# Performance work log

Hardware: AMD Instinct MI355X
Metric: run time of the kernel (lower is better)

Reference implementation:

```python
import jax, jax.numpy as jnp
from jax import lax
import numpy as np

DEPTH = 4
D_MODEL = 192
D_INNER = 384
D_STATE = 16
D_CONV = 4
DT_RANK = 12
STRIDE = 4
NUM_PATCHES = 400
L_SEQ = NUM_PATCHES + 1  # +1 cls token appended at the end
EPS = 1e-5


def _rmsnorm(x, w):
    x = x.astype(jnp.float32)
    return (x * lax.rsqrt(jnp.mean(x * x, axis=-1, keepdims=True) + EPS)) * w


def _mamba(x, in_w, cw, cb, xp_w, dtw, dtb, A_log, Dv, ow):
    # x: [B, L, D_MODEL]
    B = x.shape[0]
    xz = jnp.einsum('bld,ed->ble', x, in_w)            # [B, L, 2*D_INNER]
    u, z = jnp.split(xz, 2, axis=-1)                   # [B, L, D_INNER] each
    # causal depthwise conv over L
    u_t = jnp.transpose(u, (0, 2, 1))                  # [B, D_INNER, L]
    u_pad = jnp.pad(u_t, ((0, 0), (0, 0), (D_CONV - 1, 0)))
    conv = lax.conv_general_dilated(
        u_pad, cw[:, None, :], (1,), 'VALID',
        dimension_numbers=('NCH', 'OIH', 'NCH'),
        feature_group_count=D_INNER)                   # [B, D_INNER, L]
    u = jax.nn.silu(conv + cb[:, None])
    u = jnp.transpose(u, (0, 2, 1))                    # [B, L, D_INNER]
    xdbl = jnp.einsum('bld,ed->ble', u, xp_w)          # [B, L, 44]
    dt, Bm, Cm = jnp.split(xdbl, [DT_RANK, DT_RANK + D_STATE], axis=-1)
    dt = jax.nn.softplus(jnp.einsum('blr,dr->bld', dt, dtw) + dtb)  # [B, L, D_INNER]
    A = -jnp.exp(A_log)                                # [D_INNER, D_STATE]
    dA = jnp.exp(dt[..., None] * A)                    # [B, L, D_INNER, D_STATE]
    dBu = dt[..., None] * Bm[:, :, None, :] * u[..., None]
    h0 = jnp.zeros((B, D_INNER, D_STATE), dtype=dA.dtype)

    def step(h, inp):
        dA_t, dBu_t = inp
        h = dA_t * h + dBu_t
        return h, h

    _, hs = lax.scan(step, h0, (jnp.swapaxes(dA, 0, 1), jnp.swapaxes(dBu, 0, 1)))
    hs = jnp.swapaxes(hs, 0, 1)                        # [B, L, D_INNER, D_STATE]
    y = jnp.einsum('bldn,bln->bld', hs, Cm) + u * Dv
    y = y * jax.nn.silu(z)
    return jnp.einsum('bld,ed->ble', y, ow)            # [B, L, D_MODEL]


def _forward(imgs, patch_w, patch_b, pos_embed, cls_token, norm_w, in_proj_w,
             conv_w, conv_b, xproj_w, dt_w, dt_b, A_log, D_param, out_w,
             normf_w, head_w, head_b):
    B = imgs.shape[0]
    # StrideEmbed: non-overlapping strides of 4 bytes -> linear to embed_dim
    x = imgs.reshape(B, NUM_PATCHES, STRIDE) @ patch_w + patch_b  # [B, 400, 192]
    x = x + pos_embed[:, :-1, :]
    cls = cls_token + pos_embed[:, -1:, :]             # [1, 1, 192]
    x = jnp.concatenate([x, jnp.broadcast_to(cls, (B, 1, D_MODEL))], axis=1)
    hidden = x
    residual = None
    for i in range(DEPTH):
        residual = hidden if residual is None else hidden + residual  # fp32 residual stream
        h = _rmsnorm(residual, norm_w[i])
        hidden = _mamba(h, in_proj_w[i], conv_w[i], conv_b[i], xproj_w[i],
                        dt_w[i], dt_b[i], A_log[i], D_param[i], out_w[i])
    x = _rmsnorm(hidden + residual, normf_w)
    cls_out = x[:, -1, :]                              # [B, 192]
    logits = cls_out @ head_w.T + head_b               # [B, 1000]
    return logits


def setup_inputs() -> dict:
    key = jax.random.key(0)
    ks = jax.random.split(key, 16)
    B = 32
    rn = lambda k, s, sc: jax.random.normal(k, s, dtype=jnp.float32) * sc
    A_log = jnp.broadcast_to(jnp.log(jnp.arange(1.0, D_STATE + 1.0, dtype=jnp.float32)),
                             (DEPTH, D_INNER, D_STATE))
    return {
        'imgs': rn(ks[0], (B, 1, 40, 40), 1.0),
        'patch_w': rn(ks[1], (STRIDE, D_MODEL), 0.1),
        'patch_b': jnp.zeros((D_MODEL,), jnp.float32),
        'pos_embed': rn(ks[2], (1, L_SEQ, D_MODEL), 0.02),
        'cls_token': rn(ks[3], (1, 1, D_MODEL), 0.02),
        'norm_w': jnp.ones((DEPTH, D_MODEL), jnp.float32),
        'in_proj_w': rn(ks[4], (DEPTH, 2 * D_INNER, D_MODEL), 0.05),
        'conv_w': rn(ks[5], (DEPTH, D_INNER, D_CONV), 0.3),
        'conv_b': jnp.zeros((DEPTH, D_INNER), jnp.float32),
        'xproj_w': rn(ks[6], (DEPTH, DT_RANK + 2 * D_STATE, D_INNER), 0.05),
        'dt_w': rn(ks[7], (DEPTH, D_INNER, DT_RANK), 0.1),
        'dt_b': rn(ks[8], (DEPTH, D_INNER), 0.5) - 4.0,
        'A_log': A_log,
        'D_param': jnp.ones((DEPTH, D_INNER), jnp.float32),
        'out_w': rn(ks[9], (DEPTH, D_MODEL, D_INNER), 0.05),
        'normf_w': jnp.ones((D_MODEL,), jnp.float32),
        'head_w': rn(ks[10], (1000, D_MODEL), 0.05),
        'head_b': jnp.zeros((1000,), jnp.float32),
    }


def reference(imgs, patch_w, patch_b, pos_embed, cls_token, norm_w, in_proj_w,
              conv_w, conv_b, xproj_w, dt_w, dt_b, A_log, D_param, out_w,
              normf_w, head_w, head_b):
    return _forward(imgs, patch_w, patch_b, pos_embed, cls_token, norm_w,
                    in_proj_w, conv_w, conv_b, xproj_w, dt_w, dt_b, A_log,
                    D_param, out_w, normf_w, head_w, head_b)
```

## Files before the change

kernel.cpp:

```cpp
#include <hip/hip_runtime.h>
#include <hip/hip_bf16.h>

#define B_SZ 32
#define LSEQ 401
#define NT (B_SZ * LSEQ)
#define DM 192
#define DI 384
#define DS 16
#define EPSF 1e-5f
#define ST 40
#define STP 44
#define NCH 8
#define PQN 1376256

typedef __attribute__((ext_vector_type(8))) short short8;
typedef __attribute__((ext_vector_type(4))) float f32x4;
typedef __hip_bfloat16 bf16;

#define OFF_IMGS    0
#define OFF_PATCHW  51200
#define OFF_PATCHB  51968
#define OFF_POS     52160
#define OFF_CLS     129152
#define OFF_NORMW   129344
#define OFF_INW     130112
#define OFF_CONVW   719936
#define OFF_CONVB   726080
#define OFF_XPROJW  727616
#define OFF_DTW     795200
#define OFF_DTB     813632
#define OFF_ALOG    815168
#define OFF_DP      839744
#define OFF_OUTW    841280
#define OFF_NORMF   1136192
#define OFF_HEADW   1136384
#define OFF_HEADB   1328384
#define OFF_TOTAL   1329384

#define WB_INW   0
#define WB_XPJ   589824
#define WB_OUT   688128
#define WB_DTW   983040
#define WB_TOTAL 1032192

__device__ __forceinline__ int chunk_s(int c) { return c == 0 ? 0 : c * 50 + 1; }
__device__ __forceinline__ int chunk_e(int c) { return (c + 1) * 50 + 1; }

__device__ __forceinline__ float ldsrc(const void* p, int off, int isbf) {
  return isbf ? __bfloat162float(((const bf16*)p)[off]) : ((const float*)p)[off];
}
__device__ __forceinline__ float fast_silu(float z) {
  return z * __builtin_amdgcn_rcpf(1.f + __expf(-z));
}
__device__ __forceinline__ float fast_softplus(float x) {
  float e = __expf(x);
  return (x > 15.f) ? x : __logf(1.f + e);
}

#define DPP_ADD(x, ctrl) \
  x += __int_as_float(__builtin_amdgcn_update_dpp(0, __float_as_int(x), ctrl, 0xF, 0xF, true))
__device__ __forceinline__ float row_sum16(float x) {
  DPP_ADD(x, 0xB1);
  DPP_ADD(x, 0x4E);
  DPP_ADD(x, 0x124);
  DPP_ADD(x, 0x128);
  return x;
}

struct P18 { const void* p[18]; };

__global__ __launch_bounds__(256) void k_convwb(P18 t, float* __restrict__ fin,
                                                bf16* __restrict__ wb) {
  static const int st[19] = {OFF_IMGS, OFF_PATCHW, OFF_PATCHB, OFF_POS, OFF_CLS,
                             OFF_NORMW, OFF_INW, OFF_CONVW, OFF_CONVB, OFF_XPROJW,
                             OFF_DTW, OFF_DTB, OFF_ALOG, OFF_DP, OFF_OUTW,
                             OFF_NORMF, OFF_HEADW, OFF_HEADB, OFF_TOTAL};
  int isbf = (((const unsigned short*)t.p[5])[0] == 0x3F80) ? 1 : 0;
  int idx = blockIdx.x * 256 + threadIdx.x;
  if (idx < OFF_TOTAL) {
    int lo = 0;
#pragma unroll
    for (int i = 1; i < 18; ++i) if (idx >= st[i]) lo = i;
    fin[idx] = ldsrc(t.p[lo], idx - st[lo], isbf);
  } else if (idx < OFF_TOTAL + WB_TOTAL) {
    int j = idx - OFF_TOTAL;
    float v;
    if (j < WB_XPJ) {
      v = ldsrc(t.p[6], j, isbf);
    } else if (j < WB_OUT) {
      int i2 = j - WB_XPJ;
      int l = i2 / (64 * 384);
      int r = (i2 / 384) & 63;
      int k = i2 % 384;
      v = (r < 44) ? ldsrc(t.p[9], l * 44 * 384 + r * 384 + k, isbf) : 0.f;
    } else if (j < WB_DTW) {
      v = ldsrc(t.p[14], j - WB_OUT, isbf);
    } else {
      int i2 = j - WB_DTW;
      int l = i2 / (384 * 32);
      int r = i2 % (384 * 32);
      int d = r >> 5;
      int k = r & 31;
      v = (k < 12) ? ldsrc(t.p[10], l * 4608 + d * 12 + k, isbf) : 0.f;
    }
    wb[j] = __float2bfloat16(v);
  }
}

__device__ __forceinline__ void inproj32(const bf16 (*shb)[200],
                                         const bf16* __restrict__ Win,
                                         bf16* __restrict__ xb,
                                         bf16* __restrict__ zb,
                                         int row0, int tid) {
  int lane = tid & 63, wave = tid >> 6;
  int q = lane >> 4, mlo = lane & 15;
  short8 afrA[6], afrB[6];
#pragma unroll
  for (int kk = 0; kk < 6; ++kk) {
    afrA[kk] = *(const short8*)&shb[mlo][kk * 32 + q * 8];
    afrB[kk] = *(const short8*)&shb[16 + mlo][kk * 32 + q * 8];
  }
  const bf16* wbase = Win + (size_t)(wave * 96 + mlo) * DM + q * 8;
  short8 bc[6];
#pragma unroll
  for (int kk = 0; kk < 6; ++kk) bc[kk] = *(const short8*)(wbase + kk * 32);
#pragma unroll
  for (int j = 0; j < 6; ++j) {
    short8 bn[6];
    if (j < 5) {
#pragma unroll
      for (int kk = 0; kk < 6; ++kk)
        bn[kk] = *(const short8*)(wbase + (size_t)(j + 1) * 16 * DM + kk * 32);
    }
    f32x4 aA = {}, aB = {};
#pragma unroll
    for (int kk = 0; kk < 6; ++kk) {
      aA = __builtin_amdgcn_mfma_f32_16x16x32_bf16(afrA[kk], bc[kk], aA, 0, 0, 0);
      aB = __builtin_amdgcn_mfma_f32_16x16x32_bf16(afrB[kk], bc[kk], aB, 0, 0, 0);
    }
    int n = wave * 96 + j * 16 + mlo;
    if (n < DI) {
#pragma unroll
      for (int i = 0; i < 4; ++i) {
        xb[(size_t)(row0 + q * 4 + i) * DI + n] = __float2bfloat16(aA[i]);
        xb[(size_t)(row0 + 16 + q * 4 + i) * DI + n] = __float2bfloat16(aB[i]);
      }
    } else {
      int nz = n - DI;
#pragma unroll
      for (int i = 0; i < 4; ++i) {
        zb[(size_t)(row0 + q * 4 + i) * DI + nz] = __float2bfloat16(aA[i]);
        zb[(size_t)(row0 + 16 + q * 4 + i) * DI + nz] = __float2bfloat16(aB[i]);
      }
    }
    if (j < 5) {
#pragma unroll
      for (int kk = 0; kk < 6; ++kk) bc[kk] = bn[kk];
    }
  }
}

__global__ __launch_bounds__(512) void k_embedin(const float* __restrict__ fin,
                                                 float* __restrict__ residual,
                                                 const bf16* __restrict__ Win,
                                                 bf16* __restrict__ xb,
                                                 bf16* __restrict__ zb) {
  __shared__ bf16 shb[32][200];
  const float* imgs = fin + OFF_IMGS;
  const float* pw   = fin + OFF_PATCHW;
  const float* pb   = fin + OFF_PATCHB;
  const float* pos  = fin + OFF_POS;
  const float* cls  = fin + OFF_CLS;
  const float* nw0  = fin + OFF_NORMW;
  int tid = threadIdx.x;
  int row0 = blockIdx.x * 32;
  {
    int row = tid >> 4, g = tid & 15;
    int t = row0 + row;
    int b = t / LSEQ, l = t % LSEQ;
    float im[4];
    if (l < 400) {
#pragma unroll
      for (int s = 0; s < 4; ++s) im[s] = imgs[b * 1600 + l * 4 + s];
    }
    float rn[12], ss = 0.f;
#pragma unroll
    for (int k = 0; k < 12; ++k) {
      int col = g + 16 * k;
      float v;
      if (l < 400) {
        v = pb[col] + pos[l * DM + col];
#pragma unroll
        for (int s = 0; s < 4; ++s) v = fmaf(im[s], pw[s * DM + col], v);
      } else {
        v = cls[col] + pos[400 * DM + col];
      }
      residual[(size_t)t * DM + col] = v;
      rn[k] = v;
      ss = fmaf(v, v, ss);
    }
    ss = row_sum16(ss);
    float sres = rsqrtf(ss / (float)DM + EPSF);
#pragma unroll
    for (int k = 0; k < 12; ++k) {
      int col = g + 16 * k;
      shb[row][col] = __float2bfloat16(rn[k] * sres * nw0[col]);
    }
  }
  __syncthreads();
  inproj32(shb, Win, xb, zb, row0, tid);
}

__global__ __launch_bounds__(512) void k_xdt(const bf16* __restrict__ xb,
                                             const float* __restrict__ cw,
                                             const float* __restrict__ cb,
                                             const bf16* __restrict__ Wbf,
                                             float* __restrict__ xdbl,
                                             const bf16* __restrict__ dtwb,
                                             const float* __restrict__ dtb,
                                             bf16* __restrict__ ub,
                                             bf16* __restrict__ dto) {
  __shared__ bf16  sxt[19][392];
  __shared__ bf16  su[16][392];
  __shared__ float4 scw4[384];
  __shared__ float scb[384];
  __shared__ float sxp[2][16][48];
  __shared__ bf16  sxb[16][32];
  int row0 = blockIdx.x * 16;
  int tid = threadIdx.x;
  for (int i = tid; i < 19 * 48; i += 512) {
    int r = i / 48, c8 = i - r * 48;
    int t = row0 - 3 + r;
    if (t < 0) t = 0;
    *(short8*)&sxt[r][c8 * 8] = *(const short8*)(xb + (size_t)t * DI + c8 * 8);
  }
  for (int i = tid; i < 384; i += 512) {
    scw4[i] = ((const float4*)cw)[i];
    scb[i] = cb[i];
  }
  __syncthreads();
  for (int i = tid; i < 768; i += 512) {
    int tok = i / 48;
    int c8 = i - tok * 48;
    int d0 = c8 * 8;
    int t = row0 + tok;
    int l = t % LSEQ;
    float xr[4][8];
#pragma unroll
    for (int k = 0; k < 4; ++k) {
      short8 v = *(const short8*)&sxt[tok + k][d0];
      bool ok = (l - 3 + k) >= 0;
#pragma unroll
      for (int j = 0; j < 8; ++j) {
        unsigned int uu = ((unsigned int)(unsigned short)v[j]) << 16;
        xr[k][j] = ok ? __uint_as_float(uu) : 0.f;
      }
    }
    short8 uvv;
#pragma unroll
    for (int j = 0; j < 8; ++j) {
      float4 w = scw4[d0 + j];
      float a = scb[d0 + j];
      a = fmaf(xr[0][j], w.x, a);
      a = fmaf(xr[1][j], w.y, a);
      a = fmaf(xr[2][j], w.z, a);
      a = fmaf(xr[3][j], w.w, a);
      bf16 h = __float2bfloat16(fast_silu(a));
      uvv[j] = *reinterpret_cast<short*>(&h);
    }
    *(short8*)&su[tok][d0] = uvv;
    *(short8*)(ub + (size_t)t * DI + d0) = uvv;
  }
  __syncthreads();
  int lane = tid & 63;
  int wave = tid >> 6;
  int q = lane >> 4;
  int mlo = lane & 15;
  if (wave < 6) {
    int colw = (wave % 3) * 16;
    int kh = wave / 3;
    f32x4 acc = {};
    for (int k0 = 0; k0 < 192; k0 += 32) {
      short8 a = *(const short8*)&su[mlo][kh * 192 + k0 + q * 8];
      short8 b = *(const short8*)(Wbf + (size_t)(colw + mlo) * DI + kh * 192 + k0 + q * 8);
      acc = __builtin_amdgcn_mfma_f32_16x16x32_bf16(a, b, acc, 0, 0, 0);
    }
#pragma unroll
    for (int i = 0; i < 4; ++i) sxp[kh][q * 4 + i][colw + mlo] = acc[i];
  }
  __syncthreads();
  for (int i = tid; i < 16 * 44; i += 512) {
    int r = i / 44, c = i - r * 44;
    xdbl[(size_t)(row0 + r) * 44 + c] = sxp[0][r][c] + sxp[1][r][c];
  }
  for (int i = tid; i < 512; i += 512) {
    int tok = i >> 5, k = i & 31;
    sxb[tok][k] = __float2bfloat16(k < 12 ? sxp[0][tok][k] + sxp[1][tok][k] : 0.f);
  }
  __syncthreads();
  short8 afrag = *(const short8*)&sxb[mlo][q * 8];
#pragma unroll
  for (int jt = 0; jt < 3; ++jt) {
    int d = (wave * 3 + jt) * 16 + mlo;
    short8 bfrag = *(const short8*)(dtwb + (size_t)d * 32 + q * 8);
    f32x4 acc = {};
    acc = __builtin_amdgcn_mfma_f32_16x16x32_bf16(afrag, bfrag, acc, 0, 0, 0);
    float dtbv = dtb[d];
#pragma unroll
    for (int i = 0; i < 4; ++i)
      dto[(size_t)(row0 + q * 4 + i) * DI + d] =
          __float2bfloat16(fast_softplus(acc[i] + dtbv));
  }
}

__global__ __launch_bounds__(512) void k_scanA(const bf16* __restrict__ ub,
                                               const bf16* __restrict__ dtv,
                                               const float* __restrict__ xdbl,
                                               const float* __restrict__ A_log,
                                               float* __restrict__ Pq) {
  __shared__ float sdt[32][STP], sw[32][STP], sB[16][STP];
  int bx = blockIdx.x, b = blockIdx.y, c = blockIdx.z;
  int d0 = bx * 32;
  int tid = threadIdx.x;
  int dloc = tid >> 4, n = tid & 15;
  float A = -__expf(A_log[(d0 + dloc) * DS + n]);
  float S = 0.f, h = 0.f;
  int base = b * LSEQ;
  int lt = tid >> 5, lj = tid & 31;
  int s = chunk_s(c), e = chunk_e(c);
  for (int t0 = s; t0 < e; t0 += ST) {
    int tc = min(ST, e - t0);
    for (int tt = lt; tt < tc; tt += 16) {
      int g = base + t0 + tt;
      float dv = __bfloat162float(dtv[(size_t)g * DI + d0 + lj]);
      sdt[lj][tt] = dv;
      sw[lj][tt] = dv * __bfloat162float(ub[(size_t)g * DI + d0 + lj]);
      if (lj < 16) sB[lj][tt] = xdbl[(size_t)g * 44 + 12 + lj];
    }
    __syncthreads();
    int l4 = 0;
    for (; l4 + 4 <= tc; l4 += 4) {
      float4 dt4 = *(const float4*)&sdt[dloc][l4];
      float4 w4  = *(const float4*)&sw[dloc][l4];
      float4 B4  = *(const float4*)&sB[n][l4];
      h = fmaf(__expf(dt4.x * A), h, w4.x * B4.x);
      h = fmaf(__expf(dt4.y * A), h, w4.y * B4.y);
      h = fmaf(__expf(dt4.z * A), h, w4.z * B4.z);
      h = fmaf(__expf(dt4.w * A), h, w4.w * B4.w);
      S += dt4.x + dt4.y + dt4.z + dt4.w;
    }
    for (; l4 < tc; ++l4) {
      float dv = sdt[dloc][l4];
      h = fmaf(__expf(dv * A), h, sw[dloc][l4] * sB[n][l4]);
      S += dv;
    }
    __syncthreads();
  }
  int idx = ((c * B_SZ + b) * 12 + bx) * 512 + tid;
  Pq[idx] = __expf(A * S);
  Pq[PQN + idx] = h;
}

__global__ __launch_bounds__(512) void k_scanB(const bf16* __restrict__ zb,
                                               const bf16* __restrict__ ub,
                                               const bf16* __restrict__ dtv,
                                               const float* __restrict__ xdbl,
                                               const float* __restrict__ A_log,
                                               const float* __restrict__ Dp,
                                               const float* __restrict__ Pq,
                                               bf16* __restrict__ yb) {
  __shared__ float sdt[32][STP], sw[32][STP], sB[16][STP], sC[16][STP],
                   sz[32][STP], sy[32][STP];
  int bx = blockIdx.x, b = blockIdx.y, c = blockIdx.z;
  int d0 = bx * 32;
  int tid = threadIdx.x;
  int dloc = tid >> 4, n = tid & 15;
  float A = -__expf(A_log[(d0 + dloc) * DS + n]);
  float h = 0.f;
  for (int j = 0; j < c; ++j) {
    int idx = ((j * B_SZ + b) * 12 + bx) * 512 + tid;
    h = Pq[PQN + idx] + Pq[idx] * h;
  }
  int base = b * LSEQ;
  int lt = tid >> 5, lj = tid & 31;
  float Dvj = Dp[d0 + lj];
  int s = chunk_s(c), e = chunk_e(c);
  for (int t0 = s; t0 < e; t0 += ST) {
    int tc = min(ST, e - t0);
    for (int tt = lt; tt < tc; tt += 16) {
      int g = base + t0 + tt;
      float dv = __bfloat162float(dtv[(size_t)g * DI + d0 + lj]);
      float uv = __bfloat162float(ub[(size_t)g * DI + d0 + lj]);
      sdt[lj][tt] = dv;
      sw[lj][tt] = dv * uv;
      sy[lj][tt] = uv * Dvj;
      sz[lj][tt] = fast_silu(__bfloat162float(zb[(size_t)g * DI + d0 + lj]));
      if (lj < 32) {
        float v = xdbl[(size_t)g * 44 + 12 + lj];
        if (lj < 16) sB[lj][tt] = v;
        else         sC[lj - 16][tt] = v;
      }
    }
    __syncthreads();
    int l4 = 0;
    for (; l4 + 4 <= tc; l4 += 4) {
      float4 dt4 = *(const float4*)&sdt[dloc][l4];
      float4 w4  = *(const float4*)&sw[dloc][l4];
      float4 B4  = *(const float4*)&sB[n][l4];
      float4 C4  = *(const float4*)&sC[n][l4];
      float c0, c1, c2, c3;
      h = fmaf(__expf(dt4.x * A), h, w4.x * B4.x); c0 = row_sum16(h * C4.x);
      h = fmaf(__expf(dt4.y * A), h, w4.y * B4.y); c1 = row_sum16(h * C4.y);
      h = fmaf(__expf(dt4.z * A), h, w4.z * B4.z); c2 = row_sum16(h * C4.z);
      h = fmaf(__expf(dt4.w * A), h, w4.w * B4.w); c3 = row_sum16(h * C4.w);
      if (n == 0) {
        float4 uD4 = *(const float4*)&sy[dloc][l4];
        float4 z4  = *(const float4*)&sz[dloc][l4];
        float4 yv;
        yv.x = (c0 + uD4.x) * z4.x;
        yv.y = (c1 + uD4.y) * z4.y;
        yv.z = (c2 + uD4.z) * z4.z;
        yv.w = (c3 + uD4.w) * z4.w;
        *(float4*)&sy[dloc][l4] = yv;
      }
    }
    for (; l4 < tc; ++l4) {
      h = fmaf(__expf(sdt[dloc][l4] * A), h, sw[dloc][l4] * sB[n][l4]);
      float cc = row_sum16(h * sC[n][l4]);
      if (n == 0) sy[dloc][l4] = (cc + sy[dloc][l4]) * sz[dloc][l4];
    }
    __syncthreads();
    for (int tt = lt; tt < tc; tt += 16)
      yb[(size_t)(base + t0 + tt) * DI + d0 + lj] = __float2bfloat16(sy[lj][tt]);
    __syncthreads();
  }
}

__global__ __launch_bounds__(512) void k_outin(const bf16* __restrict__ yb,
                                               const bf16* __restrict__ Wout,
                                               float* __restrict__ residual,
                                               const float* __restrict__ nw,
                                               const bf16* __restrict__ Win,
                                               bf16* __restrict__ xb,
                                               bf16* __restrict__ zb) {
  __shared__ float sCt[32][200];
  __shared__ bf16  shb[32][200];
  int tid = threadIdx.x;
  int lane = tid & 63;
  int wave = tid >> 6;
  int row0 = blockIdx.x * 32;
  int q = lane >> 4;
  int mlo = lane & 15;
  {
    int colw = (wave & 3) * 48;
    int rg = (wave >> 2) * 16;
    const bf16* arow = yb + (size_t)(row0 + rg + mlo) * DI + q * 8;
    const bf16* brow = Wout + (size_t)(colw + mlo) * DI + q * 8;
    f32x4 acc[3] = {};
    short8 ac = *(const short8*)arow;
    short8 b0 = *(const short8*)brow;
    short8 b1 = *(const short8*)(brow + 16 * DI);
    short8 b2 = *(const short8*)(brow + 32 * DI);
#pragma unroll
    for (int k0 = 0; k0 < 384; k0 += 32) {
      short8 an, n0, n1, n2;
      if (k0 < 352) {
        an = *(const short8*)(arow + k0 + 32);
        n0 = *(const short8*)(brow + k0 + 32);
        n1 = *(const short8*)(brow + 16 * DI + k0 + 32);
        n2 = *(const short8*)(brow + 32 * DI + k0 + 32);
      }
      acc[0] = __builtin_amdgcn_mfma_f32_16x16x32_bf16(ac, b0, acc[0], 0, 0, 0);
      acc[1] = __builtin_amdgcn_mfma_f32_16x16x32_bf16(ac, b1, acc[1], 0, 0, 0);
      acc[2] = __builtin_amdgcn_mfma_f32_16x16x32_bf16(ac, b2, acc[2], 0, 0, 0);
      if (k0 < 352) { ac = an; b0 = n0; b1 = n1; b2 = n2; }
    }
#pragma unroll
    for (int j = 0; j < 3; ++j)
#pragma unroll
      for (int i = 0; i < 4; ++i) sCt[rg + q * 4 + i][colw + j * 16 + mlo] = acc[j][i];
  }
  __syncthreads();
  {
    int row = tid >> 4, g = tid & 15;
    int t = row0 + row;
    float rn[12], ss = 0.f;
#pragma unroll
    for (int k = 0; k < 12; ++k) {
      int col = g + 16 * k;
      float x = sCt[row][col] + residual[(size_t)t * DM + col];
      rn[k] = x;
      ss = fmaf(x, x, ss);
    }
    ss = row_sum16(ss);
    float sres = rsqrtf(ss / (float)DM + EPSF);
#pragma unroll
    for (int k = 0; k < 12; ++k) {
      int col = g + 16 * k;
      residual[(size_t)t * DM + col] = rn[k];
      shb[row][col] = __float2bfloat16(rn[k] * sres * nw[col]);
    }
  }
  __syncthreads();
  inproj32(shb, Win, xb, zb, row0, tid);
}

__global__ __launch_bounds__(256) void k_lastout(const bf16* __restrict__ yb,
                                                 const bf16* __restrict__ Wout,
                                                 const float* __restrict__ resIn,
                                                 float* __restrict__ clsbuf) {
  __shared__ float sCt[16][200];
  int tid = threadIdx.x;
  int lane = tid & 63;
  int wave = tid >> 6;
  int b0 = blockIdx.x * 16;
  int q = lane >> 4;
  int mlo = lane & 15;
  int colw = wave * 48;
  f32x4 acc[3] = {};
  const bf16* arow = yb + ((size_t)(b0 + mlo) * LSEQ + 400) * DI + q * 8;
  for (int k0 = 0; k0 < DI; k0 += 32) {
    short8 a = *(const short8*)(arow + k0);
#pragma unroll
    for (int j = 0; j < 3; ++j) {
      short8 b = *(const short8*)(Wout + (size_t)(colw + j * 16 + mlo) * DI + k0 + q * 8);
      acc[j] = __builtin_amdgcn_mfma_f32_16x16x32_bf16(a, b, acc[j], 0, 0, 0);
    }
  }
#pragma unroll
  for (int j = 0; j < 3; ++j)
#pragma unroll
    for (int i = 0; i < 4; ++i) sCt[q * 4 + i][colw + j * 16 + mlo] = acc[j][i];
  __syncthreads();
  int row = tid >> 4, g = tid & 15;
  int bb = b0 + row;
#pragma unroll
  for (int k = 0; k < 12; ++k) {
    int col = g + 16 * k;
    clsbuf[(size_t)bb * DM + col] =
        sCt[row][col] + resIn[((size_t)bb * LSEQ + 400) * DM + col];
  }
}

__global__ __launch_bounds__(256) void k_final(const float* __restrict__ clsbuf,
                                               const float* __restrict__ fin,
                                               const void* __restrict__ nw_raw,
                                               void* __restrict__ out) {
  const float* normf  = fin + OFF_NORMF;
  const float* head_w = fin + OFF_HEADW;
  const float* head_b = fin + OFF_HEADB;
  __shared__ float clsv[DM];
  __shared__ float partial[4];
  __shared__ float sres;
  int b = blockIdx.x;
  float r = 0.f;
  if (threadIdx.x < DM) r = clsbuf[(size_t)b * DM + threadIdx.x];
  float ss = r * r;
#pragma unroll
  for (int m = 32; m >= 1; m >>= 1) ss += __shfl_xor(ss, m, 64);
  if ((threadIdx.x & 63) == 0) partial[threadIdx.x >> 6] = ss;
  __syncthreads();
  if (threadIdx.x == 0)
    sres = rsqrtf((partial[0] + partial[1] + partial[2] + partial[3]) / (float)DM + EPSF);
  __syncthreads();
  if (threadIdx.x < DM) clsv[threadIdx.x] = r * sres * normf[threadIdx.x];
  __syncthreads();
  int isbf = (((const unsigned short*)nw_raw)[0] == 0x3F80) ? 1 : 0;
  for (int e = threadIdx.x; e < 1000; e += 256) {
    float acc = head_b[e];
    for (int k = 0; k < DM; ++k) acc = fmaf(clsv[k], head_w[e * DM + k], acc);
    if (isbf) ((bf16*)out)[b * 1000 + e] = __float2bfloat16(acc);
    else      ((float*)out)[b * 1000 + e] = acc;
  }
}

extern "C" void kernel_launch(void* const* d_in, const int* in_sizes, int n_in,
                              void* d_out, int out_size, void* d_ws, size_t ws_size,
                              hipStream_t stream) {
  char* base = (char*)d_ws;
  size_t off = 0;
  auto alloc = [&](size_t bytes) { char* p = base + off; off = (off + bytes + 255) & ~(size_t)255; return p; };
  float* fin      = (float*)alloc((size_t)OFF_TOTAL * 4);
  bf16*  wb       = (bf16*)alloc((size_t)WB_TOTAL * 2);
  float* residual = (float*)alloc((size_t)NT * DM * 4);
  bf16*  xb       = (bf16*)alloc((size_t)NT * DI * 2);
  bf16*  zb       = (bf16*)alloc((size_t)NT * DI * 2);
  bf16*  ub       = (bf16*)alloc((size_t)NT * DI * 2);
  float* xdbl     = (float*)alloc((size_t)NT * 44 * 4);
  bf16*  dtb16    = (bf16*)alloc((size_t)NT * DI * 2);
  float* Pq       = (float*)alloc((size_t)2 * PQN * 4);
  float* clsbuf   = (float*)alloc((size_t)B_SZ * DM * 4);
  bf16*  yb       = ub;

  P18 t;
  for (int i = 0; i < 18; ++i) t.p[i] = d_in[i];
  k_convwb<<<(OFF_TOTAL + WB_TOTAL + 255) / 256, 256, 0, stream>>>(t, fin, wb);

  k_embedin<<<NT / 32, 512, 0, stream>>>(fin, residual, wb + WB_INW, xb, zb);

  for (int layer = 0; layer < 4; ++layer) {
    const float* dtb = fin + OFF_DTB + layer * DI;
    const float* alog = fin + OFF_ALOG + layer * DI * DS;

    k_xdt<<<NT / 16, 512, 0, stream>>>(xb, fin + OFF_CONVW + layer * DI * 4,
                                       fin + OFF_CONVB + layer * DI,
                                       wb + WB_XPJ + layer * 64 * DI, xdbl,
                                       wb + WB_DTW + layer * 384 * 32, dtb, ub, dtb16);

    k_scanA<<<dim3(12, B_SZ, NCH - 1), 512, 0, stream>>>(ub, dtb16, xdbl, alog, Pq);
    k_scanB<<<dim3(12, B_SZ, NCH), 512, 0, stream>>>(zb, ub, dtb16, xdbl, alog,
                                                     fin + OFF_DP + layer * DI, Pq, yb);

    if (layer < 3) {
      k_outin<<<NT / 32, 512, 0, stream>>>(yb, wb + WB_OUT + layer * DM * DI, residual,
                                           fin + OFF_NORMW + (layer + 1) * DM,
                                           wb + WB_INW + (layer + 1) * 768 * DM, xb, zb);
    } else {
      k_lastout<<<2, 256, 0, stream>>>(yb, wb + WB_OUT + 3 * DM * DI, residual, clsbuf);
    }
  }
  k_final<<<B_SZ, 256, 0, stream>>>(clsbuf, fin, d_in[5], d_out);
}
```

Baseline: 594.3 us.

## Split in-projection across two blocks per row tile with residual ping-pong

The embedding and out-projection kernels now launch two blocks per 32-row tile. Each block computes either the x half or the z half of the in-projection, so every wave handles 48 output columns instead of 96 and the grid doubles. This is meant to spread 401 large blocks more evenly over the CUs. The price is that the out-projection, residual add and RMSNorm are computed twice per tile, once in each block. Because both blocks read the residual, it is now double-buffered (read one buffer, write the other) to avoid a race.

```diff
diff --git a/kernel.cpp b/kernel.cpp
--- a/kernel.cpp
+++ b/kernel.cpp
@@ -107,11 +107,10 @@
   }
 }
 
-__device__ __forceinline__ void inproj32(const bf16 (*shb)[200],
-                                         const bf16* __restrict__ Win,
-                                         bf16* __restrict__ xb,
-                                         bf16* __restrict__ zb,
-                                         int row0, int tid) {
+__device__ __forceinline__ void inproj_half(const bf16 (*shb)[200],
+                                            const bf16* __restrict__ Win,
+                                            bf16* __restrict__ dst,
+                                            int half, int row0, int tid) {
   int lane = tid & 63, wave = tid >> 6;
   int q = lane >> 4, mlo = lane & 15;
   short8 afrA[6], afrB[6];
@@ -120,14 +119,13 @@
     afrA[kk] = *(const short8*)&shb[mlo][kk * 32 + q * 8];
     afrB[kk] = *(const short8*)&shb[16 + mlo][kk * 32 + q * 8];
   }
-  const bf16* wbase = Win + (size_t)(wave * 96 + mlo) * DM + q * 8;
-  short8 bc[6];
+  const bf16* wbase = Win + (size_t)(half * 384 + wave * 48 + mlo) * DM + q * 8;
+  short8 bc[6], bn[6];
 #pragma unroll
   for (int kk = 0; kk < 6; ++kk) bc[kk] = *(const short8*)(wbase + kk * 32);
 #pragma unroll
-  for (int j = 0; j < 6; ++j) {
-    short8 bn[6];
-    if (j < 5) {
+  for (int j = 0; j < 3; ++j) {
+    if (j < 2) {
 #pragma unroll
       for (int kk = 0; kk < 6; ++kk)
         bn[kk] = *(const short8*)(wbase + (size_t)(j + 1) * 16 * DM + kk * 32);
@@ -138,22 +136,13 @@
       aA = __builtin_amdgcn_mfma_f32_16x16x32_bf16(afrA[kk], bc[kk], aA, 0, 0, 0);
       aB = __builtin_amdgcn_mfma_f32_16x16x32_bf16(afrB[kk], bc[kk], aB, 0, 0, 0);
     }
-    int n = wave * 96 + j * 16 + mlo;
-    if (n < DI) {
-#pragma unroll
-      for (int i = 0; i < 4; ++i) {
-        xb[(size_t)(row0 + q * 4 + i) * DI + n] = __float2bfloat16(aA[i]);
-        xb[(size_t)(row0 + 16 + q * 4 + i) * DI + n] = __float2bfloat16(aB[i]);
-      }
-    } else {
-      int nz = n - DI;
-#pragma unroll
-      for (int i = 0; i < 4; ++i) {
-        zb[(size_t)(row0 + q * 4 + i) * DI + nz] = __float2bfloat16(aA[i]);
-        zb[(size_t)(row0 + 16 + q * 4 + i) * DI + nz] = __float2bfloat16(aB[i]);
-      }
-    }
-    if (j < 5) {
+    int n = wave * 48 + j * 16 + mlo;
+#pragma unroll
+    for (int i = 0; i < 4; ++i) {
+      dst[(size_t)(row0 + q * 4 + i) * DI + n] = __float2bfloat16(aA[i]);
+      dst[(size_t)(row0 + 16 + q * 4 + i) * DI + n] = __float2bfloat16(aB[i]);
+    }
+    if (j < 2) {
 #pragma unroll
       for (int kk = 0; kk < 6; ++kk) bc[kk] = bn[kk];
     }
@@ -173,7 +162,8 @@
   const float* cls  = fin + OFF_CLS;
   const float* nw0  = fin + OFF_NORMW;
   int tid = threadIdx.x;
-  int row0 = blockIdx.x * 32;
+  int half = blockIdx.x & 1;
+  int row0 = (blockIdx.x >> 1) * 32;
   {
     int row = tid >> 4, g = tid & 15;
     int t = row0 + row;
@@ -208,7 +198,7 @@
     }
   }
   __syncthreads();
-  inproj32(shb, Win, xb, zb, row0, tid);
+  inproj_half(shb, Win, half ? zb : xb, half, row0, tid);
 }
 
 __global__ __launch_bounds__(512) void k_xdt(const bf16* __restrict__ xb,
@@ -438,7 +428,8 @@
 
 __global__ __launch_bounds__(512) void k_outin(const bf16* __restrict__ yb,
                                                const bf16* __restrict__ Wout,
-                                               float* __restrict__ residual,
+                                               const float* __restrict__ residIn,
+                                               float* __restrict__ residOut,
                                                const float* __restrict__ nw,
                                                const bf16* __restrict__ Win,
                                                bf16* __restrict__ xb,
@@ -448,7 +439,8 @@
   int tid = threadIdx.x;
   int lane = tid & 63;
   int wave = tid >> 6;
-  int row0 = blockIdx.x * 32;
+  int half = blockIdx.x & 1;
+  int row0 = (blockIdx.x >> 1) * 32;
   int q = lane >> 4;
   int mlo = lane & 15;
   {
@@ -488,7 +480,7 @@
 #pragma unroll
     for (int k = 0; k < 12; ++k) {
       int col = g + 16 * k;
-      float x = sCt[row][col] + residual[(size_t)t * DM + col];
+      float x = sCt[row][col] + residIn[(size_t)t * DM + col];
       rn[k] = x;
       ss = fmaf(x, x, ss);
     }
@@ -497,12 +489,12 @@
 #pragma unroll
     for (int k = 0; k < 12; ++k) {
       int col = g + 16 * k;
-      residual[(size_t)t * DM + col] = rn[k];
+      residOut[(size_t)t * DM + col] = rn[k];
       shb[row][col] = __float2bfloat16(rn[k] * sres * nw[col]);
     }
   }
   __syncthreads();
-  inproj32(shb, Win, xb, zb, row0, tid);
+  inproj_half(shb, Win, half ? zb : xb, half, row0, tid);
 }
 
 __global__ __launch_bounds__(256) void k_lastout(const bf16* __restrict__ yb,
@@ -582,7 +574,8 @@
   auto alloc = [&](size_t bytes) { char* p = base + off; off = (off + bytes + 255) & ~(size_t)255; return p; };
   float* fin      = (float*)alloc((size_t)OFF_TOTAL * 4);
   bf16*  wb       = (bf16*)alloc((size_t)WB_TOTAL * 2);
-  float* residual = (float*)alloc((size_t)NT * DM * 4);
+  float* residA   = (float*)alloc((size_t)NT * DM * 4);
+  float* residB   = (float*)alloc((size_t)NT * DM * 4);
   bf16*  xb       = (bf16*)alloc((size_t)NT * DI * 2);
   bf16*  zb       = (bf16*)alloc((size_t)NT * DI * 2);
   bf16*  ub       = (bf16*)alloc((size_t)NT * DI * 2);
@@ -596,7 +589,7 @@
   for (int i = 0; i < 18; ++i) t.p[i] = d_in[i];
   k_convwb<<<(OFF_TOTAL + WB_TOTAL + 255) / 256, 256, 0, stream>>>(t, fin, wb);
 
-  k_embedin<<<NT / 32, 512, 0, stream>>>(fin, residual, wb + WB_INW, xb, zb);
+  k_embedin<<<NT / 16, 512, 0, stream>>>(fin, residA, wb + WB_INW, xb, zb);
 
   for (int layer = 0; layer < 4; ++layer) {
     const float* dtb = fin + OFF_DTB + layer * DI;
@@ -612,11 +605,13 @@
                                                      fin + OFF_DP + layer * DI, Pq, yb);
 
     if (layer < 3) {
-      k_outin<<<NT / 32, 512, 0, stream>>>(yb, wb + WB_OUT + layer * DM * DI, residual,
+      const float* rin = (layer & 1) ? residB : residA;
+      float* rout      = (layer & 1) ? residA : residB;
+      k_outin<<<NT / 16, 512, 0, stream>>>(yb, wb + WB_OUT + layer * DM * DI, rin, rout,
                                            fin + OFF_NORMW + (layer + 1) * DM,
                                            wb + WB_INW + (layer + 1) * 768 * DM, xb, zb);
     } else {
-      k_lastout<<<2, 256, 0, stream>>>(yb, wb + WB_OUT + 3 * DM * DI, residual, clsbuf);
+      k_lastout<<<2, 256, 0, stream>>>(yb, wb + WB_OUT + 3 * DM * DI, residB, clsbuf);
     }
   }
   k_final<<<B_SZ, 256, 0, stream>>>(clsbuf, fin, d_in[5], d_out);
```

After: 659.4 us. +11.0%, slower.
